# Kernel optimization log

Hardware: AMD Instinct MI355X
Metric: run time of the kernel (lower is better)

## Reference

```python
import jax, jax.numpy as jnp
import numpy as np

HADAMARD_DIM = 4096  # power of 2 -> had_rem_dim is None, rem_dim = 1


def _fwht(x):
    """Fast Walsh-Hadamard transform along last dim (natural/Sylvester order).

    x: [B, n] with n a power of 2. Returns x @ H_n (unnormalized).
    Mirrors QuaRot's recursive butterfly: at each stage, pairs are split into
    (a+b) and (a-b) halves. log2(n) stages, each O(n) work per row.
    """
    bsz, n = x.shape
    steps = int(np.log2(n))
    u = x[:, :, None]  # [B, n, 1]
    m = n
    for _ in range(steps):  # fixed-trip loop over log2(n) stages, jit-friendly
        u = u.reshape(bsz, m // 2, 2, -1)
        a = u[:, :, 0, :]
        b = u[:, :, 1, :]
        u = jnp.concatenate([a + b, a - b], axis=-1)  # [B, m//2, 2k]
        m //= 2
    return u.reshape(bsz, n)


def matmul_hadU(x):
    """QuaRot matmul_hadU for power-of-2 dim: normalized FWHT, 1/sqrt(n)."""
    n = x.shape[-1]
    flat = x.reshape(-1, n)
    out = _fwht(flat) * (1.0 / np.sqrt(n))
    return out.reshape(x.shape).astype(x.dtype)


def setup_inputs() -> dict:
    key = jax.random.key(0)
    x = jax.random.normal(key, (8192, HADAMARD_DIM), dtype=jnp.float32)
    return {"x": x}


def reference(x):
    # FWHT.forward: x -> matmul_hadU_cuda(x, None, 1) -> cast back to x.dtype
    return matmul_hadU(x)
```

## Files before the change

### kernel.cpp

```cpp
#include <hip/hip_runtime.h>


#define N        4096
#define THREADS  64
#define TSTR     68
#define LDS_FLOATS (64 * TSTR)

__device__ __forceinline__ void fwht64(float v[64]) {
#pragma unroll
    for (int s = 1; s < 64; s <<= 1) {
#pragma unroll
        for (int k = 0; k < 64; k++) {
            if ((k & s) == 0) {
                float a = v[k];
                float b = v[k + s];
                v[k]     = a + b;
                v[k + s] = a - b;
            }
        }
    }
}

__global__ __launch_bounds__(THREADS)
void FWHT_83476984365427_kernel(const float* __restrict__ x,
                                float* __restrict__ out,
                                int nrows) {
    __shared__ float tile[LDS_FLOATS];

    const int row = blockIdx.x;
    if (row >= nrows) return;

    const float* __restrict__ xr  = x   + (size_t)row * N;
    float* __restrict__       otr = out + (size_t)row * N;
    const int l = threadIdx.x;

    float v[64];

    {
        const float4* xv = (const float4*)xr + (size_t)l * 16;
#pragma unroll
        for (int c = 0; c < 16; c++) {
            float4 f = xv[c];
            v[4 * c + 0] = f.x;
            v[4 * c + 1] = f.y;
            v[4 * c + 2] = f.z;
            v[4 * c + 3] = f.w;
        }
    }

    fwht64(v);

    {
        float* dst = &tile[l * TSTR];
#pragma unroll
        for (int c = 0; c < 16; c++) {
            float4 f;
            f.x = v[4 * c + 0];
            f.y = v[4 * c + 1];
            f.z = v[4 * c + 2];
            f.w = v[4 * c + 3];
            *(float4*)(dst + 4 * c) = f;
        }
    }
    __syncthreads();

#pragma unroll
    for (int m = 0; m < 64; m++) v[m] = tile[m * TSTR + l];

    fwht64(v);

    const float scale = 1.0f / 64.0f;
#pragma unroll
    for (int m = 0; m < 64; m++) otr[m * 64 + l] = v[m] * scale;
}

extern "C" void kernel_launch(void* const* d_in, const int* in_sizes, int n_in,
                              void* d_out, int out_size, void* d_ws, size_t ws_size,
                              hipStream_t stream) {
    (void)n_in; (void)d_ws; (void)ws_size; (void)out_size;
    const float* x = (const float*)d_in[0];
    float* out = (float*)d_out;
    const int nrows = in_sizes[0] / N;
    dim3 grid(nrows);
    dim3 block(THREADS);
    FWHT_83476984365427_kernel<<<grid, block, 0, stream>>>(x, out, nrows);
}
```

Baseline: 230.1 us.

## Stage input rows into LDS via global_load_lds with XOR-swizzled layout

Input loads now go straight from global memory into LDS through the async global_load_lds builtin, using coalesced per-wavefront accesses, instead of each thread doing strided float4 loads of its own 256-byte chunk. The padded tile is replaced by an unpadded 4096-float buffer with an XOR swizzle on float4 columns, so both the row-wise and the column-wise LDS accesses avoid bank conflicts. The cost is an extra barrier plus a vmcnt wait before compute, and correctness depends on the swizzle indexing matching the builtin's per-lane LDS placement.

```diff
diff --git a/kernel.cpp b/kernel.cpp
--- a/kernel.cpp
+++ b/kernel.cpp
@@ -3,8 +3,7 @@
 
 #define N        4096
 #define THREADS  64
-#define TSTR     68
-#define LDS_FLOATS (64 * TSTR)
+#define LDS_FLOATS 4096
 
 __device__ __forceinline__ void fwht64(float v[64]) {
 #pragma unroll
@@ -25,22 +24,38 @@
 void FWHT_83476984365427_kernel(const float* __restrict__ x,
                                 float* __restrict__ out,
                                 int nrows) {
-    __shared__ float tile[LDS_FLOATS];
+    __shared__ float lds[LDS_FLOATS];
 
     const int row = blockIdx.x;
     if (row >= nrows) return;
 
     const float* __restrict__ xr  = x   + (size_t)row * N;
     float* __restrict__       otr = out + (size_t)row * N;
-    const int l = threadIdx.x;
+    const int l  = threadIdx.x;
+    const int lh = l >> 4;
+    const int ls = l & 15;
+
+#pragma unroll
+    for (int i = 0; i < 16; i++) {
+        const int hi = 4 * i + lh;
+        const int hm = 4 * (i & 3) + lh;
+        const int c  = ls ^ hm;
+        const float* src = xr + hi * 64 + c * 4;
+        __builtin_amdgcn_global_load_lds(
+            (const __attribute__((address_space(1))) void*)src,
+            (__attribute__((address_space(3))) void*)(&lds[i * 256]),
+            16, 0, 0);
+    }
+    asm volatile("s_waitcnt vmcnt(0)" ::: "memory");
+    __syncthreads();
 
     float v[64];
 
     {
-        const float4* xv = (const float4*)xr + (size_t)l * 16;
+        const float* rowp = &lds[l * 64];
 #pragma unroll
         for (int c = 0; c < 16; c++) {
-            float4 f = xv[c];
+            float4 f = *(const float4*)(rowp + ((c ^ ls) << 2));
             v[4 * c + 0] = f.x;
             v[4 * c + 1] = f.y;
             v[4 * c + 2] = f.z;
@@ -51,7 +66,7 @@
     fwht64(v);
 
     {
-        float* dst = &tile[l * TSTR];
+        float* rowp = &lds[l * 64];
 #pragma unroll
         for (int c = 0; c < 16; c++) {
             float4 f;
@@ -59,13 +74,23 @@
             f.y = v[4 * c + 1];
             f.z = v[4 * c + 2];
             f.w = v[4 * c + 3];
-            *(float4*)(dst + 4 * c) = f;
+            *(float4*)(rowp + ((c ^ ls) << 2)) = f;
         }
     }
     __syncthreads();
 
+    {
+        const int l2 = l >> 2;
+        const int j  = l & 3;
 #pragma unroll
-    for (int m = 0; m < 64; m++) v[m] = tile[m * TSTR + l];
+        for (int ml = 0; ml < 16; ml++) {
+            const int off = ((l2 ^ ml) << 2) + j;
+#pragma unroll
+            for (int mh = 0; mh < 4; mh++) {
+                v[mh * 16 + ml] = lds[(mh * 16 + ml) * 64 + off];
+            }
+        }
+    }
 
     fwht64(v);
 
```

New measurement: 229.3 us. About the same (-0.4%).

## Replace LDS transpose with wave shuffles and coalesced float4 row access

Applied to the files above, without the earlier changes.

Each wavefront now handles one row with interleaved float4 loads and stores so global accesses are coalesced. The middle six butterfly stages run across lanes with xor shuffles instead of an LDS transpose. Blocks hold four waves to raise occupancy. The cost is many cross-lane shuffle operations, 64 per stage over 6 stages.

```diff
diff --git a/kernel.cpp b/kernel.cpp
--- a/kernel.cpp
+++ b/kernel.cpp
@@ -2,13 +2,32 @@
 
 
 #define N        4096
-#define THREADS  64
-#define TSTR     68
-#define LDS_FLOATS (64 * TSTR)
+#define THREADS  256
 
-__device__ __forceinline__ void fwht64(float v[64]) {
+__global__ __launch_bounds__(THREADS)
+void FWHT_83476984365427_kernel(const float* __restrict__ x,
+                                float* __restrict__ out,
+                                int nrows) {
+    const int wid = blockIdx.x * (THREADS / 64) + (threadIdx.x >> 6);
+    if (wid >= nrows) return;
+    const int l = threadIdx.x & 63;
+
+    const float* __restrict__ xr  = x   + (size_t)wid * N;
+    float* __restrict__       otr = out + (size_t)wid * N;
+
+    float v[64];
+
 #pragma unroll
-    for (int s = 1; s < 64; s <<= 1) {
+    for (int i = 0; i < 16; i++) {
+        float4 f = *(const float4*)(xr + i * 256 + l * 4);
+        v[4 * i + 0] = f.x;
+        v[4 * i + 1] = f.y;
+        v[4 * i + 2] = f.z;
+        v[4 * i + 3] = f.w;
+    }
+
+#pragma unroll
+    for (int s = 1; s < 4; s <<= 1) {
 #pragma unroll
         for (int k = 0; k < 64; k++) {
             if ((k & s) == 0) {
@@ -19,59 +38,40 @@
             }
         }
     }
-}
 
-__global__ __launch_bounds__(THREADS)
-void FWHT_83476984365427_kernel(const float* __restrict__ x,
-                                float* __restrict__ out,
-                                int nrows) {
-    __shared__ float tile[LDS_FLOATS];
-
-    const int row = blockIdx.x;
-    if (row >= nrows) return;
-
-    const float* __restrict__ xr  = x   + (size_t)row * N;
-    float* __restrict__       otr = out + (size_t)row * N;
-    const int l = threadIdx.x;
-
-    float v[64];
-
-    {
-        const float4* xv = (const float4*)xr + (size_t)l * 16;
 #pragma unroll
-        for (int c = 0; c < 16; c++) {
-            float4 f = xv[c];
-            v[4 * c + 0] = f.x;
-            v[4 * c + 1] = f.y;
-            v[4 * c + 2] = f.z;
-            v[4 * c + 3] = f.w;
+    for (int m = 1; m < 64; m <<= 1) {
+        const float sgn = (l & m) ? -1.0f : 1.0f;
+#pragma unroll
+        for (int r = 0; r < 64; r++) {
+            float p = __shfl_xor(v[r], m, 64);
+            v[r] = fmaf(sgn, v[r], p);
         }
     }
 
-    fwht64(v);
-
-    {
-        float* dst = &tile[l * TSTR];
 #pragma unroll
-        for (int c = 0; c < 16; c++) {
-            float4 f;
-            f.x = v[4 * c + 0];
-            f.y = v[4 * c + 1];
-            f.z = v[4 * c + 2];
-            f.w = v[4 * c + 3];
-            *(float4*)(dst + 4 * c) = f;
+    for (int s = 4; s < 64; s <<= 1) {
+#pragma unroll
+        for (int k = 0; k < 64; k++) {
+            if ((k & s) == 0) {
+                float a = v[k];
+                float b = v[k + s];
+                v[k]     = a + b;
+                v[k + s] = a - b;
+            }
         }
     }
-    __syncthreads();
-
-#pragma unroll
-    for (int m = 0; m < 64; m++) v[m] = tile[m * TSTR + l];
-
-    fwht64(v);
 
     const float scale = 1.0f / 64.0f;
 #pragma unroll
-    for (int m = 0; m < 64; m++) otr[m * 64 + l] = v[m] * scale;
+    for (int i = 0; i < 16; i++) {
+        float4 f;
+        f.x = v[4 * i + 0] * scale;
+        f.y = v[4 * i + 1] * scale;
+        f.z = v[4 * i + 2] * scale;
+        f.w = v[4 * i + 3] * scale;
+        *(float4*)(otr + i * 256 + l * 4) = f;
+    }
 }
 
 extern "C" void kernel_launch(void* const* d_in, const int* in_sizes, int n_in,
@@ -81,7 +81,8 @@
     const float* x = (const float*)d_in[0];
     float* out = (float*)d_out;
     const int nrows = in_sizes[0] / N;
-    dim3 grid(nrows);
+    const int wpb = THREADS / 64;
+    dim3 grid((nrows + wpb - 1) / wpb);
     dim3 block(THREADS);
     FWHT_83476984365427_kernel<<<grid, block, 0, stream>>>(x, out, nrows);
 }
```

New measurement: 234.2 us. About the same (+1.8%).
